# Optimization experiments

Measured on AMD Instinct MI355X. Metric: run time of the kernel, lower is better.

## Reference

```python
import jax, jax.numpy as jnp
import numpy as np

N = 50000        # nodes
E = 800000       # edges (avg degree 16)
IN = 128         # n_feat
C0, H0 = 32, 4   # layer0: out_channels, heads (concat -> 128)
C1, H1 = 32, 1   # layer1: out_channels, heads (mean)
NEG_SLOPE = 0.2


def setup_inputs() -> dict:
    key = jax.random.key(0)
    ks = jax.random.split(key, 16)
    def p(k, shape, fan):
        return jax.random.normal(k, shape, jnp.float32) / np.float32(np.sqrt(fan))
    x = jax.random.normal(ks[0], (N, IN), jnp.float32)
    edge_index = jax.random.randint(ks[1], (2, E), 0, N, dtype=jnp.int32)
    return {
        "x": x,
        "edge_index": edge_index,
        # layer 0 GATConv: in=128 -> 4 heads x 32, concat
        "W0": p(ks[2], (H0 * C0, IN), IN),
        "att_src0": p(ks[3], (H0, C0), C0),
        "att_dst0": p(ks[4], (H0, C0), C0),
        "bias0": jnp.zeros((H0 * C0,), jnp.float32),
        "linW0": p(ks[5], (H0 * C0, IN), IN),
        "linb0": jnp.zeros((H0 * C0,), jnp.float32),
        # layer 1 GATConv: in=128 -> 1 head x 32, mean
        "W1": p(ks[6], (H1 * C1, H0 * C0), H0 * C0),
        "att_src1": p(ks[7], (H1, C1), C1),
        "att_dst1": p(ks[8], (H1, C1), C1),
        "bias1": jnp.zeros((C1,), jnp.float32),
        "linW1": p(ks[9], (C1, H0 * C0), H0 * C0),
        "linb1": jnp.zeros((C1,), jnp.float32),
    }


def gat_conv(x, src, dst, W, att_src, att_dst, bias, concat):
    """PyG-style GATConv (self-loops already appended to src/dst)."""
    n = x.shape[0]
    H, C = att_src.shape
    h = (x @ W.T).reshape(n, H, C)                       # [N,H,C]
    a_src = jnp.einsum('nhc,hc->nh', h, att_src)          # [N,H]
    a_dst = jnp.einsum('nhc,hc->nh', h, att_dst)          # [N,H]
    e = jax.nn.leaky_relu(a_src[src] + a_dst[dst], NEG_SLOPE)  # [E,H]
    # segment softmax over incoming edges of each dst node
    m = jax.ops.segment_max(e, dst, num_segments=n)       # [N,H]
    ex = jnp.exp(e - m[dst])
    denom = jax.ops.segment_sum(ex, dst, num_segments=n)  # [N,H]
    alpha = ex / (denom[dst] + 1e-16)                     # [E,H]
    out = jax.ops.segment_sum(h[src] * alpha[:, :, None], dst, num_segments=n)  # [N,H,C]
    out = out.reshape(n, H * C) if concat else out.mean(axis=1)
    return out + bias


def reference(x, edge_index, W0, att_src0, att_dst0, bias0, linW0, linb0,
              W1, att_src1, att_dst1, bias1, linW1, linb1):
    n = x.shape[0]
    loop = jnp.arange(n, dtype=edge_index.dtype)
    src = jnp.concatenate([edge_index[0], loop])  # add self-loops
    dst = jnp.concatenate([edge_index[1], loop])
    # layer 0: conv + linear skip, then ELU (eval mode -> dropout is a no-op)
    h = gat_conv(x, src, dst, W0, att_src0, att_dst0, bias0, True) + x @ linW0.T + linb0
    h = jax.nn.elu(h)
    # layer 1 (last): conv + linear skip, no activation
    out = gat_conv(h, src, dst, W1, att_src1, att_dst1, bias1, False) + h @ linW1.T + linb1
    return out
```

## Files before the change

### kernel.cpp

```cpp
#include <hip/hip_runtime.h>
#include <hip/hip_bf16.h>


typedef __attribute__((ext_vector_type(8))) short bf8_t;
typedef __attribute__((ext_vector_type(4))) float f4_t;

#define NBUCK 256
#define BCAP  8192

__device__ inline short f2bf(float f) {
    return (short)__builtin_bit_cast(unsigned short, __float2bfloat16(f));
}
__device__ inline float blo(unsigned int p) { return __uint_as_float(p << 16); }
__device__ inline float bhi(unsigned int p) { return __uint_as_float(p & 0xffff0000u); }
__device__ inline float lrexp(float e) {
    e = (e > 0.f) ? e : 0.2f * e;
    return __expf(e);
}

__global__ void k_init(const float* __restrict__ W0, const float* __restrict__ lW0,
                       const float* __restrict__ W1, const float* __restrict__ lW1,
                       const float* __restrict__ b0, const float* __restrict__ lb0,
                       const float* __restrict__ b1, const float* __restrict__ lb1,
                       short* __restrict__ Wp0, short* __restrict__ lWp0,
                       short* __restrict__ Wp1, short* __restrict__ lWp1,
                       float* __restrict__ bc0, float* __restrict__ bc1,
                       int* __restrict__ gcur) {
    int i = blockIdx.x * blockDim.x + threadIdx.x;
    if (i < NBUCK) gcur[i] = i * BCAP;
    if (i < 16384) {
        int j = i & 7, lane = (i >> 3) & 63, kc = i >> 9;
        int kb = kc & 3, ct = kc >> 2;
        int src = (ct * 16 + (lane & 15)) * 128 + kb * 32 + (lane >> 4) * 8 + j;
        Wp0[i]  = f2bf(W0[src]);
        lWp0[i] = f2bf(lW0[src]);
    }
    if (i < 4096) {
        int j = i & 7, lane = (i >> 3) & 63, kc = i >> 9;
        int kb = kc & 3, ct = kc >> 2;
        int src = (ct * 16 + (lane & 15)) * 128 + kb * 32 + (lane >> 4) * 8 + j;
        Wp1[i]  = f2bf(W1[src]);
        lWp1[i] = f2bf(lW1[src]);
    }
    if (i < 128) bc0[i] = b0[i] + lb0[i];
    else if (i < 160) bc1[i - 128] = b1[i - 128] + lb1[i - 128];
}


__global__ __launch_bounds__(256) void k_bucket(
    const int* __restrict__ ei, int* __restrict__ gcur,
    unsigned int* __restrict__ bucketed, int E, int T) {
    __shared__ int hist[NBUCK];
    __shared__ int gbase[NBUCK];
    int tid = threadIdx.x;
    hist[tid] = 0;
    __syncthreads();
    int base = blockIdx.x * 2048;
    unsigned int pk[8]; int rk[8]; int bk[8];
    #pragma unroll
    for (int j = 0; j < 8; j++) {
        int e = base + j * 256 + tid;
        if (e < T) {
            int src, dst;
            if (e < E) { src = ei[e]; dst = ei[E + e]; }
            else       { src = e - E; dst = src; }
            int b = dst >> 8;
            pk[j] = ((unsigned int)dst << 16) | (unsigned int)src;
            bk[j] = b;
            rk[j] = atomicAdd(&hist[b], 1);
        } else bk[j] = -1;
    }
    __syncthreads();
    int h = hist[tid];
    if (h > 0) gbase[tid] = atomicAdd(&gcur[tid], h);
    __syncthreads();
    #pragma unroll
    for (int j = 0; j < 8; j++)
        if (bk[j] >= 0)
            bucketed[gbase[bk[j]] + rk[j]] = pk[j];
}

__global__ void k_bscan(const int* __restrict__ gcur, int* __restrict__ bbase,
                        int* __restrict__ rowstart, int n) {
    __shared__ int buf[NBUCK];
    int t = threadIdx.x;
    int v = gcur[t] - t * BCAP;
    buf[t] = v;
    __syncthreads();
    for (int off = 1; off < NBUCK; off <<= 1) {
        int tv = (t >= off) ? buf[t - off] : 0;
        __syncthreads();
        buf[t] += tv;
        __syncthreads();
    }
    bbase[t] = buf[t] - v;
    if (t == NBUCK - 1) rowstart[n] = buf[t];
}

__global__ __launch_bounds__(256) void k_fill2(
    const unsigned int* __restrict__ bucketed, const int* __restrict__ gcur,
    const int* __restrict__ bbase, int* __restrict__ rowstart,
    unsigned short* __restrict__ esrc, int N) {
    __shared__ int hist[256];
    __shared__ int incl[256];
    int b = blockIdx.x, t = threadIdx.x;
    int nodebase = b << 8;
    int used = gcur[b] - b * BCAP;
    const unsigned int* bk = bucketed + (size_t)b * BCAP;
    hist[t] = 0;
    __syncthreads();
    for (int i = t; i < used; i += 256)
        atomicAdd(&hist[(bk[i] >> 16) - nodebase], 1);
    __syncthreads();
    int v = hist[t];
    incl[t] = v;
    __syncthreads();
    for (int off = 1; off < 256; off <<= 1) {
        int tv = (t >= off) ? incl[t - off] : 0;
        __syncthreads();
        incl[t] += tv;
        __syncthreads();
    }
    int myexcl = incl[t] - v;
    int rbase = bbase[b];
    int node = nodebase + t;
    if (node < N) rowstart[node] = rbase + myexcl;
    __syncthreads();
    hist[t] = myexcl;
    __syncthreads();
    for (int i = t; i < used; i += 256) {
        unsigned int p = bk[i];
        int pos = atomicAdd(&hist[(p >> 16) - nodebase], 1);
        esrc[rbase + pos] = (unsigned short)(p & 0xffffu);
    }
}


#define TSTR 136

__global__ __launch_bounds__(256) void k_gemm0(
    const float* __restrict__ x,
    const short* __restrict__ Wp0, const short* __restrict__ lWp0,
    const float* __restrict__ as0, const float* __restrict__ ad0,
    __hip_bfloat16* __restrict__ h0, __hip_bfloat16* __restrict__ skipb,
    float* __restrict__ a0s, float* __restrict__ a0d, int N) {
    __shared__ short tile[4][16 * TSTR];
    int wv = threadIdx.x >> 6, lane = threadIdx.x & 63;
    int rowbase = blockIdx.x * 64 + wv * 16;
    int m = lane & 15, q = lane >> 4;
    int arow = rowbase + m; if (arow >= N) arow = N - 1;
    bf8_t a[4];
    #pragma unroll
    for (int kb = 0; kb < 4; kb++) {
        const float4* px = (const float4*)(x + (size_t)arow * 128 + kb * 32 + q * 8);
        float4 lo = px[0], hi = px[1];
        bf8_t f;
        f[0] = f2bf(lo.x); f[1] = f2bf(lo.y); f[2] = f2bf(lo.z); f[3] = f2bf(lo.w);
        f[4] = f2bf(hi.x); f[5] = f2bf(hi.y); f[6] = f2bf(hi.z); f[7] = f2bf(hi.w);
        a[kb] = f;
    }
    float sacc[4][4], dacc[4][4];
    #pragma unroll
    for (int h = 0; h < 4; h++)
        #pragma unroll
        for (int r = 0; r < 4; r++) { sacc[h][r] = 0.f; dacc[h][r] = 0.f; }
    short* tl = tile[wv];
    int r4 = lane >> 2, qt = lane & 3;
    int drow = rowbase + r4;

    #pragma unroll
    for (int ct = 0; ct < 8; ct++) {
        f4_t acc = {0.f, 0.f, 0.f, 0.f};
        #pragma unroll
        for (int kb = 0; kb < 4; kb++) {
            bf8_t b = *(const bf8_t*)(Wp0 + (((ct * 4 + kb) * 64 + lane) << 3));
            acc = __builtin_amdgcn_mfma_f32_16x16x32_bf16(a[kb], b, acc, 0, 0, 0);
        }
        int hd = ct >> 1;
        float ws = as0[ct * 16 + m], wd = ad0[ct * 16 + m];
        #pragma unroll
        for (int r = 0; r < 4; r++) {
            sacc[hd][r] += acc[r] * ws;
            dacc[hd][r] += acc[r] * wd;
            tl[(q * 4 + r) * TSTR + ct * 16 + m] = f2bf(acc[r]);
        }
    }
    if (drow < N) {
        short* dst = (short*)h0 + (size_t)drow * 128 + qt * 32;
        const short* srcp = tl + r4 * TSTR + qt * 32;
        #pragma unroll
        for (int s = 0; s < 4; s++)
            *(uint4*)(dst + s * 8) = *(const uint4*)(srcp + s * 8);
    }

    #pragma unroll
    for (int ct = 0; ct < 8; ct++) {
        f4_t acc = {0.f, 0.f, 0.f, 0.f};
        #pragma unroll
        for (int kb = 0; kb < 4; kb++) {
            bf8_t b = *(const bf8_t*)(lWp0 + (((ct * 4 + kb) * 64 + lane) << 3));
            acc = __builtin_amdgcn_mfma_f32_16x16x32_bf16(a[kb], b, acc, 0, 0, 0);
        }
        #pragma unroll
        for (int r = 0; r < 4; r++)
            tl[(q * 4 + r) * TSTR + ct * 16 + m] = f2bf(acc[r]);
    }
    if (drow < N) {
        short* dst = (short*)skipb + (size_t)drow * 128 + qt * 32;
        const short* srcp = tl + r4 * TSTR + qt * 32;
        #pragma unroll
        for (int s = 0; s < 4; s++)
            *(uint4*)(dst + s * 8) = *(const uint4*)(srcp + s * 8);
    }

    #pragma unroll
    for (int h = 0; h < 4; h++)
        #pragma unroll
        for (int r = 0; r < 4; r++) {
            float s = sacc[h][r], d = dacc[h][r];
            #pragma unroll
            for (int off = 1; off < 16; off <<= 1) {
                s += __shfl_xor(s, off);
                d += __shfl_xor(d, off);
            }
            sacc[h][r] = s; dacc[h][r] = d;
        }
    if (m < 4) {
        #pragma unroll
        for (int r = 0; r < 4; r++) {
            int row = rowbase + q * 4 + r;
            if (row < N) {
                float sv = (m == 0) ? sacc[0][r] : (m == 1) ? sacc[1][r]
                         : (m == 2) ? sacc[2][r] : sacc[3][r];
                float dv = (m == 0) ? dacc[0][r] : (m == 1) ? dacc[1][r]
                         : (m == 2) ? dacc[2][r] : dacc[3][r];
                a0s[row * 4 + m] = sv;
                a0d[row * 4 + m] = dv;
            }
        }
    }
}


__global__ __launch_bounds__(256) void k_gemm1(
    const __hip_bfloat16* __restrict__ hin,
    const short* __restrict__ Wp1, const short* __restrict__ lWp1,
    const float* __restrict__ as1, const float* __restrict__ ad1,
    __hip_bfloat16* __restrict__ h1, float* __restrict__ skipb ,
    float* __restrict__ a1s, float* __restrict__ a1d, int N) {
    __shared__ short th[4][16 * 40];
    __shared__ float ts[4][16 * 36];
    int wv = threadIdx.x >> 6, lane = threadIdx.x & 63;
    int rowbase = blockIdx.x * 64 + wv * 16;
    int m = lane & 15, q = lane >> 4;
    int arow = rowbase + m; if (arow >= N) arow = N - 1;
    const short* xs = (const short*)hin;
    bf8_t a[4];
    #pragma unroll
    for (int kb = 0; kb < 4; kb++)
        a[kb] = *(const bf8_t*)(xs + (size_t)arow * 128 + kb * 32 + q * 8);
    float sacc[4], dacc[4];
    #pragma unroll
    for (int r = 0; r < 4; r++) { sacc[r] = 0.f; dacc[r] = 0.f; }
    short* tlh = th[wv];
    float* tls = ts[wv];
    int r4 = lane >> 2, qt = lane & 3;
    int drow = rowbase + r4;

    #pragma unroll
    for (int ct = 0; ct < 2; ct++) {
        f4_t acc = {0.f, 0.f, 0.f, 0.f};
        #pragma unroll
        for (int kb = 0; kb < 4; kb++) {
            bf8_t b = *(const bf8_t*)(Wp1 + (((ct * 4 + kb) * 64 + lane) << 3));
            acc = __builtin_amdgcn_mfma_f32_16x16x32_bf16(a[kb], b, acc, 0, 0, 0);
        }
        float ws = as1[ct * 16 + m], wd = ad1[ct * 16 + m];
        #pragma unroll
        for (int r = 0; r < 4; r++) {
            sacc[r] += acc[r] * ws;
            dacc[r] += acc[r] * wd;
            tlh[(q * 4 + r) * 40 + ct * 16 + m] = f2bf(acc[r]);
        }
    }
    #pragma unroll
    for (int ct = 0; ct < 2; ct++) {
        f4_t acc = {0.f, 0.f, 0.f, 0.f};
        #pragma unroll
        for (int kb = 0; kb < 4; kb++) {
            bf8_t b = *(const bf8_t*)(lWp1 + (((ct * 4 + kb) * 64 + lane) << 3));
            acc = __builtin_amdgcn_mfma_f32_16x16x32_bf16(a[kb], b, acc, 0, 0, 0);
        }
        #pragma unroll
        for (int r = 0; r < 4; r++)
            tls[(q * 4 + r) * 36 + ct * 16 + m] = acc[r];
    }
    if (drow < N) {
        *(uint4*)((short*)h1 + (size_t)drow * 32 + qt * 8) =
            *(const uint4*)(tlh + r4 * 40 + qt * 8);
        float* dst = skipb + (size_t)drow * 32 + qt * 8;
        const float* srcp = tls + r4 * 36 + qt * 8;
        *(uint4*)(dst) = *(const uint4*)(srcp);
        *(uint4*)(dst + 4) = *(const uint4*)(srcp + 4);
    }
    #pragma unroll
    for (int r = 0; r < 4; r++) {
        float s = sacc[r], d = dacc[r];
        #pragma unroll
        for (int off = 1; off < 16; off <<= 1) {
            s += __shfl_xor(s, off);
            d += __shfl_xor(d, off);
        }
        if (m == 0) {
            int row = rowbase + q * 4 + r;
            if (row < N) { a1s[row] = s; a1d[row] = d; }
        }
    }
}


__global__ __launch_bounds__(256) void k_agg0(
    const int* __restrict__ rowstart, const unsigned short* __restrict__ esrc,
    const unsigned int* __restrict__ h0u,
    const float* __restrict__ a0s, const float* __restrict__ a0d,
    const float* __restrict__ bc0,
    unsigned int* __restrict__ h1in_u,
    int n) {
    int node = (blockIdx.x * 256 + threadIdx.x) >> 6;
    int lane = threadIdx.x & 63;
    if (node >= n) return;
    int g = lane >> 4, t = lane & 15, hd = t >> 2;
    float ad = a0d[node * 4 + hd];
    int s0 = rowstart[node], s1 = rowstart[node + 1];
    float den = 0.f;
    float acc[8];
    #pragma unroll
    for (int k = 0; k < 8; k++) acc[k] = 0.f;
    int i = s0 + g;
    for (; i + 4 < s1; i += 8) {
        int sA = esrc[i], sB = esrc[i + 4];
        float eA = a0s[sA * 4 + hd] + ad;
        float eB = a0s[sB * 4 + hd] + ad;
        uint4 pA = *(const uint4*)(h0u + (size_t)sA * 64 + t * 4);
        uint4 pB = *(const uint4*)(h0u + (size_t)sB * 64 + t * 4);
        float wA = lrexp(eA), wB = lrexp(eB);
        den += wA + wB;
        acc[0] += wA * blo(pA.x) + wB * blo(pB.x);
        acc[1] += wA * bhi(pA.x) + wB * bhi(pB.x);
        acc[2] += wA * blo(pA.y) + wB * blo(pB.y);
        acc[3] += wA * bhi(pA.y) + wB * bhi(pB.y);
        acc[4] += wA * blo(pA.z) + wB * blo(pB.z);
        acc[5] += wA * bhi(pA.z) + wB * bhi(pB.z);
        acc[6] += wA * blo(pA.w) + wB * blo(pB.w);
        acc[7] += wA * bhi(pA.w) + wB * bhi(pB.w);
    }
    for (; i < s1; i += 4) {
        int s = esrc[i];
        float wv = lrexp(a0s[s * 4 + hd] + ad);
        uint4 p = *(const uint4*)(h0u + (size_t)s * 64 + t * 4);
        den += wv;
        acc[0] += wv * blo(p.x); acc[1] += wv * bhi(p.x);
        acc[2] += wv * blo(p.y); acc[3] += wv * bhi(p.y);
        acc[4] += wv * blo(p.z); acc[5] += wv * bhi(p.z);
        acc[6] += wv * blo(p.w); acc[7] += wv * bhi(p.w);
    }
    #pragma unroll
    for (int k = 0; k < 8; k++) {
        acc[k] += __shfl_xor(acc[k], 16);
        acc[k] += __shfl_xor(acc[k], 32);
    }
    den += __shfl_xor(den, 16);
    den += __shfl_xor(den, 32);
    if (g == 0) {
        float inv = 1.0f / (den + 1e-16f);
        uint4 sp = *(const uint4*)(h1in_u + (size_t)node * 64 + t * 4);
        int c0 = t * 8;
        float o[8];
        o[0] = acc[0] * inv + blo(sp.x) + bc0[c0 + 0];
        o[1] = acc[1] * inv + bhi(sp.x) + bc0[c0 + 1];
        o[2] = acc[2] * inv + blo(sp.y) + bc0[c0 + 2];
        o[3] = acc[3] * inv + bhi(sp.y) + bc0[c0 + 3];
        o[4] = acc[4] * inv + blo(sp.z) + bc0[c0 + 4];
        o[5] = acc[5] * inv + bhi(sp.z) + bc0[c0 + 5];
        o[6] = acc[6] * inv + blo(sp.w) + bc0[c0 + 6];
        o[7] = acc[7] * inv + bhi(sp.w) + bc0[c0 + 7];
        #pragma unroll
        for (int k = 0; k < 8; k++)
            o[k] = (o[k] > 0.f) ? o[k] : (__expf(o[k]) - 1.f);
        uint4 res;
        res.x = (unsigned int)(unsigned short)f2bf(o[0]) | ((unsigned int)(unsigned short)f2bf(o[1]) << 16);
        res.y = (unsigned int)(unsigned short)f2bf(o[2]) | ((unsigned int)(unsigned short)f2bf(o[3]) << 16);
        res.z = (unsigned int)(unsigned short)f2bf(o[4]) | ((unsigned int)(unsigned short)f2bf(o[5]) << 16);
        res.w = (unsigned int)(unsigned short)f2bf(o[6]) | ((unsigned int)(unsigned short)f2bf(o[7]) << 16);
        *(uint4*)(h1in_u + (size_t)node * 64 + t * 4) = res;
    }
}

__global__ __launch_bounds__(256) void k_agg1(
    const int* __restrict__ rowstart, const unsigned short* __restrict__ esrc,
    const __hip_bfloat16* __restrict__ h1,
    const float* __restrict__ a1s, const float* __restrict__ a1d,
    const float* __restrict__ bc1,
    float* __restrict__ out, int n) {
    int node = (blockIdx.x * 256 + threadIdx.x) >> 6;
    int lane = threadIdx.x & 63;
    if (node >= n) return;
    int g = lane >> 4, t = lane & 15;
    float ad = a1d[node];
    int s0 = rowstart[node], s1 = rowstart[node + 1];
    const unsigned int* h1w = (const unsigned int*)h1;
    float den = 0.f, acc0 = 0.f, acc1 = 0.f;
    int i = s0 + g;
    for (; i + 4 < s1; i += 8) {
        int sA = esrc[i], sB = esrc[i + 4];
        float eA = a1s[sA] + ad, eB = a1s[sB] + ad;
        unsigned int pA = h1w[(size_t)sA * 16 + t];
        unsigned int pB = h1w[(size_t)sB * 16 + t];
        float wA = lrexp(eA), wB = lrexp(eB);
        den += wA + wB;
        acc0 += wA * blo(pA) + wB * blo(pB);
        acc1 += wA * bhi(pA) + wB * bhi(pB);
    }
    for (; i < s1; i += 4) {
        int s = esrc[i];
        float wv = lrexp(a1s[s] + ad);
        unsigned int p = h1w[(size_t)s * 16 + t];
        den += wv; acc0 += wv * blo(p); acc1 += wv * bhi(p);
    }
    acc0 += __shfl_xor(acc0, 16); acc0 += __shfl_xor(acc0, 32);
    acc1 += __shfl_xor(acc1, 16); acc1 += __shfl_xor(acc1, 32);
    den  += __shfl_xor(den, 16);  den  += __shfl_xor(den, 32);
    if (g == 0) {
        float inv = 1.0f / (den + 1e-16f);
        int c0 = t * 2;
        size_t idx = (size_t)node * 32 + c0;
        float2 sk = *(const float2*)(out + idx);
        float2 r;
        r.x = acc0 * inv + sk.x + bc1[c0];
        r.y = acc1 * inv + sk.y + bc1[c0 + 1];
        *(float2*)(out + idx) = r;
    }
}


extern "C" void kernel_launch(void* const* d_in, const int* in_sizes, int n_in,
                              void* d_out, int out_size, void* d_ws, size_t ws_size,
                              hipStream_t stream) {
    const float* x   = (const float*)d_in[0];
    const int*   ei  = (const int*)d_in[1];
    const float* W0  = (const float*)d_in[2];
    const float* as0 = (const float*)d_in[3];
    const float* ad0 = (const float*)d_in[4];
    const float* b0  = (const float*)d_in[5];
    const float* lW0 = (const float*)d_in[6];
    const float* lb0 = (const float*)d_in[7];
    const float* W1  = (const float*)d_in[8];
    const float* as1 = (const float*)d_in[9];
    const float* ad1 = (const float*)d_in[10];
    const float* b1  = (const float*)d_in[11];
    const float* lW1 = (const float*)d_in[12];
    const float* lb1 = (const float*)d_in[13];
    float* out = (float*)d_out;

    const int N = in_sizes[0] / 128;
    const int E = in_sizes[1] / 2;
    const int T = E + N;
    const int NBK = (N + 255) >> 8;

    char* w = (char*)d_ws;
    auto alloc = [&](size_t bytes) -> char* {
        char* p = w; w += (bytes + 255) / 256 * 256; return p;
    };
    int* rowstart  = (int*)alloc((size_t)(N + 1) * 4);
    int* gcur      = (int*)alloc(NBUCK * 4);
    int* bbase     = (int*)alloc(NBUCK * 4);
    unsigned int* bucketed = (unsigned int*)alloc((size_t)NBUCK * BCAP * 4);
    unsigned short* esrc = (unsigned short*)alloc((size_t)T * 2);
    float* aS      = (float*)alloc((size_t)N * 4 * 4);
    float* aD      = (float*)alloc((size_t)N * 4 * 4);
    __hip_bfloat16* hbuf = (__hip_bfloat16*)alloc((size_t)N * 128 * 2);
    __hip_bfloat16* h1in = (__hip_bfloat16*)alloc((size_t)N * 128 * 2);
    short* Wp0  = (short*)alloc(16384 * 2);
    short* lWp0 = (short*)alloc(16384 * 2);
    short* Wp1  = (short*)alloc(4096 * 2);
    short* lWp1 = (short*)alloc(4096 * 2);
    float* bc0  = (float*)alloc(128 * 4);
    float* bc1  = (float*)alloc(32 * 4);

    k_init<<<64, 256, 0, stream>>>(W0, lW0, W1, lW1, b0, lb0, b1, lb1,
                                   Wp0, lWp0, Wp1, lWp1, bc0, bc1, gcur);
    k_bucket<<<(T + 2047) / 2048, 256, 0, stream>>>(ei, gcur, bucketed, E, T);
    k_bscan<<<1, NBUCK, 0, stream>>>(gcur, bbase, rowstart, N);
    k_fill2<<<NBK, 256, 0, stream>>>(bucketed, gcur, bbase, rowstart, esrc, N);

    k_gemm0<<<(N + 63) / 64, 256, 0, stream>>>(x, Wp0, lWp0, as0, ad0,
                                               hbuf, h1in, aS, aD, N);
    k_agg0<<<(N + 3) / 4, 256, 0, stream>>>(rowstart, esrc, (const unsigned int*)hbuf,
                                            aS, aD, bc0, (unsigned int*)h1in, N);
    k_gemm1<<<(N + 63) / 64, 256, 0, stream>>>(h1in, Wp1, lWp1, as1, ad1,
                                               hbuf, out, aS, aD, N);
    k_agg1<<<(N + 3) / 4, 256, 0, stream>>>(rowstart, esrc, hbuf, aS, aD,
                                            bc1, out, N);
}
```

Baseline: 225.9 us.

## Fuse CSR build kernels with init/gemm0 and deepen gather unroll in aggregations

Merges weight packing into the bucketing kernel and folds the bucket scan into the last-finishing bucket block using an atomic done counter. The CSR fill blocks are co-launched with the gemm0 blocks in one grid, and a tiny kernel zeroes the counters. Together this cuts the launch count and lets independent work overlap. The aggregation loops also process four edges per iteration instead of two, so more gathers are in flight. The cost is extra register pressure and a threadfence/atomic last-block pattern.

```diff
diff --git a/kernel.cpp b/kernel.cpp
--- a/kernel.cpp
+++ b/kernel.cpp
@@ -18,44 +18,51 @@
     return __expf(e);
 }
 
-__global__ void k_init(const float* __restrict__ W0, const float* __restrict__ lW0,
-                       const float* __restrict__ W1, const float* __restrict__ lW1,
-                       const float* __restrict__ b0, const float* __restrict__ lb0,
-                       const float* __restrict__ b1, const float* __restrict__ lb1,
-                       short* __restrict__ Wp0, short* __restrict__ lWp0,
-                       short* __restrict__ Wp1, short* __restrict__ lWp1,
-                       float* __restrict__ bc0, float* __restrict__ bc1,
-                       int* __restrict__ gcur) {
-    int i = blockIdx.x * blockDim.x + threadIdx.x;
-    if (i < NBUCK) gcur[i] = i * BCAP;
-    if (i < 16384) {
-        int j = i & 7, lane = (i >> 3) & 63, kc = i >> 9;
-        int kb = kc & 3, ct = kc >> 2;
-        int src = (ct * 16 + (lane & 15)) * 128 + kb * 32 + (lane >> 4) * 8 + j;
-        Wp0[i]  = f2bf(W0[src]);
-        lWp0[i] = f2bf(lW0[src]);
-    }
-    if (i < 4096) {
-        int j = i & 7, lane = (i >> 3) & 63, kc = i >> 9;
-        int kb = kc & 3, ct = kc >> 2;
-        int src = (ct * 16 + (lane & 15)) * 128 + kb * 32 + (lane >> 4) * 8 + j;
-        Wp1[i]  = f2bf(W1[src]);
-        lWp1[i] = f2bf(lW1[src]);
-    }
-    if (i < 128) bc0[i] = b0[i] + lb0[i];
-    else if (i < 160) bc1[i - 128] = b1[i - 128] + lb1[i - 128];
-}
-
-
-__global__ __launch_bounds__(256) void k_bucket(
-    const int* __restrict__ ei, int* __restrict__ gcur,
-    unsigned int* __restrict__ bucketed, int E, int T) {
+__global__ void k_gz(int* __restrict__ gcur, int* __restrict__ done) {
+    int i = threadIdx.x;
+    gcur[i] = i * BCAP;
+    if (i == 0) *done = 0;
+}
+
+__global__ __launch_bounds__(256) void k_initbucket(
+    const int* __restrict__ ei,
+    const float* __restrict__ W0, const float* __restrict__ lW0,
+    const float* __restrict__ W1, const float* __restrict__ lW1,
+    const float* __restrict__ b0, const float* __restrict__ lb0,
+    const float* __restrict__ b1, const float* __restrict__ lb1,
+    short* __restrict__ Wp0, short* __restrict__ lWp0,
+    short* __restrict__ Wp1, short* __restrict__ lWp1,
+    float* __restrict__ bc0, float* __restrict__ bc1,
+    int* __restrict__ gcur, int* __restrict__ done,
+    int* __restrict__ bbase, int* __restrict__ rowstart,
+    unsigned int* __restrict__ bucketed, int E, int T, int N) {
     __shared__ int hist[NBUCK];
     __shared__ int gbase[NBUCK];
+    __shared__ int lastflag;
     int tid = threadIdx.x;
+
+    if (blockIdx.x < 64) {
+        int i = blockIdx.x * 256 + tid;
+        {
+            int j = i & 7, lane = (i >> 3) & 63, kc = i >> 9;
+            int kb = kc & 3, ct = kc >> 2;
+            int src = (ct * 16 + (lane & 15)) * 128 + kb * 32 + (lane >> 4) * 8 + j;
+            Wp0[i]  = f2bf(W0[src]);
+            lWp0[i] = f2bf(lW0[src]);
+            if (i < 4096) {
+                Wp1[i]  = f2bf(W1[src]);
+                lWp1[i] = f2bf(lW1[src]);
+            }
+        }
+        if (i < 128) bc0[i] = b0[i] + lb0[i];
+        else if (i < 160) bc1[i - 128] = b1[i - 128] + lb1[i - 128];
+        return;
+    }
+
+    int bb = blockIdx.x - 64;
     hist[tid] = 0;
     __syncthreads();
-    int base = blockIdx.x * 2048;
+    int base = bb * 2048;
     unsigned int pk[8]; int rk[8]; int bk[8];
     #pragma unroll
     for (int j = 0; j < 8; j++) {
@@ -78,75 +85,79 @@
     for (int j = 0; j < 8; j++)
         if (bk[j] >= 0)
             bucketed[gbase[bk[j]] + rk[j]] = pk[j];
-}
-
-__global__ void k_bscan(const int* __restrict__ gcur, int* __restrict__ bbase,
-                        int* __restrict__ rowstart, int n) {
-    __shared__ int buf[NBUCK];
-    int t = threadIdx.x;
-    int v = gcur[t] - t * BCAP;
-    buf[t] = v;
+
+    __threadfence();
+    __syncthreads();
+    if (tid == 0) lastflag = (atomicAdd(done, 1) == (int)(gridDim.x - 64) - 1);
+    __syncthreads();
+    if (!lastflag) return;
+    int v = atomicAdd(&gcur[tid], 0) - tid * BCAP;
+    hist[tid] = v;
     __syncthreads();
     for (int off = 1; off < NBUCK; off <<= 1) {
-        int tv = (t >= off) ? buf[t - off] : 0;
-        __syncthreads();
-        buf[t] += tv;
-        __syncthreads();
-    }
-    bbase[t] = buf[t] - v;
-    if (t == NBUCK - 1) rowstart[n] = buf[t];
-}
-
-__global__ __launch_bounds__(256) void k_fill2(
+        int tv = (tid >= off) ? hist[tid - off] : 0;
+        __syncthreads();
+        hist[tid] += tv;
+        __syncthreads();
+    }
+    bbase[tid] = hist[tid] - v;
+    if (tid == NBUCK - 1) rowstart[N] = hist[tid];
+}
+
+
+#define TSTR 136
+
+__global__ __launch_bounds__(256) void k_fillgemm0(
     const unsigned int* __restrict__ bucketed, const int* __restrict__ gcur,
     const int* __restrict__ bbase, int* __restrict__ rowstart,
-    unsigned short* __restrict__ esrc, int N) {
-    __shared__ int hist[256];
-    __shared__ int incl[256];
-    int b = blockIdx.x, t = threadIdx.x;
-    int nodebase = b << 8;
-    int used = gcur[b] - b * BCAP;
-    const unsigned int* bk = bucketed + (size_t)b * BCAP;
-    hist[t] = 0;
-    __syncthreads();
-    for (int i = t; i < used; i += 256)
-        atomicAdd(&hist[(bk[i] >> 16) - nodebase], 1);
-    __syncthreads();
-    int v = hist[t];
-    incl[t] = v;
-    __syncthreads();
-    for (int off = 1; off < 256; off <<= 1) {
-        int tv = (t >= off) ? incl[t - off] : 0;
-        __syncthreads();
-        incl[t] += tv;
-        __syncthreads();
-    }
-    int myexcl = incl[t] - v;
-    int rbase = bbase[b];
-    int node = nodebase + t;
-    if (node < N) rowstart[node] = rbase + myexcl;
-    __syncthreads();
-    hist[t] = myexcl;
-    __syncthreads();
-    for (int i = t; i < used; i += 256) {
-        unsigned int p = bk[i];
-        int pos = atomicAdd(&hist[(p >> 16) - nodebase], 1);
-        esrc[rbase + pos] = (unsigned short)(p & 0xffffu);
-    }
-}
-
-
-#define TSTR 136
-
-__global__ __launch_bounds__(256) void k_gemm0(
+    unsigned short* __restrict__ esrc,
     const float* __restrict__ x,
     const short* __restrict__ Wp0, const short* __restrict__ lWp0,
     const float* __restrict__ as0, const float* __restrict__ ad0,
     __hip_bfloat16* __restrict__ h0, __hip_bfloat16* __restrict__ skipb,
     float* __restrict__ a0s, float* __restrict__ a0d, int N) {
+    __shared__ int ihist[256];
+    __shared__ int incl[256];
     __shared__ short tile[4][16 * TSTR];
+    int NBK = (N + 255) >> 8;
+
+    if ((int)blockIdx.x < NBK) {
+        int b = blockIdx.x, t = threadIdx.x;
+        int nodebase = b << 8;
+        int used = gcur[b] - b * BCAP;
+        const unsigned int* bk = bucketed + (size_t)b * BCAP;
+        ihist[t] = 0;
+        __syncthreads();
+        for (int i = t; i < used; i += 256)
+            atomicAdd(&ihist[(bk[i] >> 16) - nodebase], 1);
+        __syncthreads();
+        int v = ihist[t];
+        incl[t] = v;
+        __syncthreads();
+        for (int off = 1; off < 256; off <<= 1) {
+            int tv = (t >= off) ? incl[t - off] : 0;
+            __syncthreads();
+            incl[t] += tv;
+            __syncthreads();
+        }
+        int myexcl = incl[t] - v;
+        int rbase = bbase[b];
+        int node = nodebase + t;
+        if (node < N) rowstart[node] = rbase + myexcl;
+        __syncthreads();
+        ihist[t] = myexcl;
+        __syncthreads();
+        for (int i = t; i < used; i += 256) {
+            unsigned int p = bk[i];
+            int pos = atomicAdd(&ihist[(p >> 16) - nodebase], 1);
+            esrc[rbase + pos] = (unsigned short)(p & 0xffffu);
+        }
+        return;
+    }
+
+    int bx = blockIdx.x - NBK;
     int wv = threadIdx.x >> 6, lane = threadIdx.x & 63;
-    int rowbase = blockIdx.x * 64 + wv * 16;
+    int rowbase = bx * 64 + wv * 16;
     int m = lane & 15, q = lane >> 4;
     int arow = rowbase + m; if (arow >= N) arow = N - 1;
     bf8_t a[4];
@@ -337,22 +348,23 @@
     #pragma unroll
     for (int k = 0; k < 8; k++) acc[k] = 0.f;
     int i = s0 + g;
-    for (; i + 4 < s1; i += 8) {
-        int sA = esrc[i], sB = esrc[i + 4];
-        float eA = a0s[sA * 4 + hd] + ad;
-        float eB = a0s[sB * 4 + hd] + ad;
-        uint4 pA = *(const uint4*)(h0u + (size_t)sA * 64 + t * 4);
-        uint4 pB = *(const uint4*)(h0u + (size_t)sB * 64 + t * 4);
-        float wA = lrexp(eA), wB = lrexp(eB);
-        den += wA + wB;
-        acc[0] += wA * blo(pA.x) + wB * blo(pB.x);
-        acc[1] += wA * bhi(pA.x) + wB * bhi(pB.x);
-        acc[2] += wA * blo(pA.y) + wB * blo(pB.y);
-        acc[3] += wA * bhi(pA.y) + wB * bhi(pB.y);
-        acc[4] += wA * blo(pA.z) + wB * blo(pB.z);
-        acc[5] += wA * bhi(pA.z) + wB * bhi(pB.z);
-        acc[6] += wA * blo(pA.w) + wB * blo(pB.w);
-        acc[7] += wA * bhi(pA.w) + wB * bhi(pB.w);
+    for (; i + 12 < s1; i += 16) {
+        int sE[4]; float e[4]; uint4 p[4];
+        #pragma unroll
+        for (int j = 0; j < 4; j++) sE[j] = esrc[i + 4 * j];
+        #pragma unroll
+        for (int j = 0; j < 4; j++) e[j] = a0s[sE[j] * 4 + hd] + ad;
+        #pragma unroll
+        for (int j = 0; j < 4; j++) p[j] = *(const uint4*)(h0u + (size_t)sE[j] * 64 + t * 4);
+        #pragma unroll
+        for (int j = 0; j < 4; j++) {
+            float wgt = lrexp(e[j]);
+            den += wgt;
+            acc[0] += wgt * blo(p[j].x); acc[1] += wgt * bhi(p[j].x);
+            acc[2] += wgt * blo(p[j].y); acc[3] += wgt * bhi(p[j].y);
+            acc[4] += wgt * blo(p[j].z); acc[5] += wgt * bhi(p[j].z);
+            acc[6] += wgt * blo(p[j].w); acc[7] += wgt * bhi(p[j].w);
+        }
     }
     for (; i < s1; i += 4) {
         int s = esrc[i];
@@ -411,15 +423,21 @@
     const unsigned int* h1w = (const unsigned int*)h1;
     float den = 0.f, acc0 = 0.f, acc1 = 0.f;
     int i = s0 + g;
-    for (; i + 4 < s1; i += 8) {
-        int sA = esrc[i], sB = esrc[i + 4];
-        float eA = a1s[sA] + ad, eB = a1s[sB] + ad;
-        unsigned int pA = h1w[(size_t)sA * 16 + t];
-        unsigned int pB = h1w[(size_t)sB * 16 + t];
-        float wA = lrexp(eA), wB = lrexp(eB);
-        den += wA + wB;
-        acc0 += wA * blo(pA) + wB * blo(pB);
-        acc1 += wA * bhi(pA) + wB * bhi(pB);
+    for (; i + 12 < s1; i += 16) {
+        int sE[4]; float e[4]; unsigned int p[4];
+        #pragma unroll
+        for (int j = 0; j < 4; j++) sE[j] = esrc[i + 4 * j];
+        #pragma unroll
+        for (int j = 0; j < 4; j++) e[j] = a1s[sE[j]] + ad;
+        #pragma unroll
+        for (int j = 0; j < 4; j++) p[j] = h1w[(size_t)sE[j] * 16 + t];
+        #pragma unroll
+        for (int j = 0; j < 4; j++) {
+            float wgt = lrexp(e[j]);
+            den += wgt;
+            acc0 += wgt * blo(p[j]);
+            acc1 += wgt * bhi(p[j]);
+        }
     }
     for (; i < s1; i += 4) {
         int s = esrc[i];
@@ -465,7 +483,8 @@
     const int N = in_sizes[0] / 128;
     const int E = in_sizes[1] / 2;
     const int T = E + N;
-    const int NBK = (N + 255) >> 8;
+    const int NBK  = (N + 255) >> 8;
+    const int NBBK = (T + 2047) / 2048;
 
     char* w = (char*)d_ws;
     auto alloc = [&](size_t bytes) -> char* {
@@ -473,6 +492,7 @@
     };
     int* rowstart  = (int*)alloc((size_t)(N + 1) * 4);
     int* gcur      = (int*)alloc(NBUCK * 4);
+    int* done      = (int*)alloc(4);
     int* bbase     = (int*)alloc(NBUCK * 4);
     unsigned int* bucketed = (unsigned int*)alloc((size_t)NBUCK * BCAP * 4);
     unsigned short* esrc = (unsigned short*)alloc((size_t)T * 2);
@@ -487,14 +507,15 @@
     float* bc0  = (float*)alloc(128 * 4);
     float* bc1  = (float*)alloc(32 * 4);
 
-    k_init<<<64, 256, 0, stream>>>(W0, lW0, W1, lW1, b0, lb0, b1, lb1,
-                                   Wp0, lWp0, Wp1, lWp1, bc0, bc1, gcur);
-    k_bucket<<<(T + 2047) / 2048, 256, 0, stream>>>(ei, gcur, bucketed, E, T);
-    k_bscan<<<1, NBUCK, 0, stream>>>(gcur, bbase, rowstart, N);
-    k_fill2<<<NBK, 256, 0, stream>>>(bucketed, gcur, bbase, rowstart, esrc, N);
-
-    k_gemm0<<<(N + 63) / 64, 256, 0, stream>>>(x, Wp0, lWp0, as0, ad0,
-                                               hbuf, h1in, aS, aD, N);
+    k_gz<<<1, NBUCK, 0, stream>>>(gcur, done);
+    k_initbucket<<<64 + NBBK, 256, 0, stream>>>(ei, W0, lW0, W1, lW1,
+                                                b0, lb0, b1, lb1,
+                                                Wp0, lWp0, Wp1, lWp1, bc0, bc1,
+                                                gcur, done, bbase, rowstart,
+                                                bucketed, E, T, N);
+    k_fillgemm0<<<NBK + (N + 63) / 64, 256, 0, stream>>>(
+        bucketed, gcur, bbase, rowstart, esrc,
+        x, Wp0, lWp0, as0, ad0, hbuf, h1in, aS, aD, N);
     k_agg0<<<(N + 3) / 4, 256, 0, stream>>>(rowstart, esrc, (const unsigned int*)hbuf,
                                             aS, aD, bc0, (unsigned int*)h1in, N);
     k_gemm1<<<(N + 63) / 64, 256, 0, stream>>>(h1in, Wp1, lWp1, as1, ad1,
```

Result: slower. 266.8 us (+18.1%).
